# Performance work log

Hardware: AMD Instinct MI355X
Metric: run time of the kernel (lower is better)

## Reference

```python
import jax, jax.numpy as jnp
import numpy as np

NUM_AGENTS = 16


def setup_inputs() -> dict:
    key = jax.random.key(0)
    ks = jax.random.split(key, 9)
    B, N, C = 64, 1024, 512
    w_scale = 1.0 / np.sqrt(C)  # keep pre-softmax logits in a sane range
    return {
        "x": jax.random.normal(ks[0], (B, N, C), dtype=jnp.float32),
        "Wq": jax.random.normal(ks[1], (C, C), dtype=jnp.float32) * w_scale,
        "bq": jax.random.normal(ks[2], (C,), dtype=jnp.float32) * 0.02,
        "Wk": jax.random.normal(ks[3], (C, C), dtype=jnp.float32) * w_scale,
        "bk": jax.random.normal(ks[4], (C,), dtype=jnp.float32) * 0.02,
        "Wv": jax.random.normal(ks[5], (C, C), dtype=jnp.float32) * w_scale,
        "bv": jax.random.normal(ks[6], (C,), dtype=jnp.float32) * 0.02,
        "Wo": jax.random.normal(ks[7], (C, C), dtype=jnp.float32) * w_scale,
        "bo": jax.random.normal(ks[8], (C,), dtype=jnp.float32) * 0.02,
    }


def reference(x, Wq, bq, Wk, bk, Wv, bv, Wo, bo):
    B, N, C = x.shape
    M = NUM_AGENTS
    scale = C ** (-0.5)
    # torch nn.Linear: y = x @ W.T + b
    Q = jnp.einsum('bnc,dc->bnd', x, Wq) + bq  # [B,N,C]
    K = jnp.einsum('bnc,dc->bnd', x, Wk) + bk
    V = jnp.einsum('bnc,dc->bnd', x, Wv) + bv
    # adaptive_avg_pool1d over token dim; N % M == 0 -> mean over groups of N//M
    A = Q.reshape(B, M, N // M, C).mean(axis=2)  # [B,M,C]
    # stage 1: softmax(Q A^T)
    agent_tokens = jax.nn.softmax(jnp.einsum('bnc,bmc->bnm', Q, A) * scale, axis=-1)  # [B,N,M]
    # stage 2: softmax(A K^T) V
    agent_features = jax.nn.softmax(jnp.einsum('bmc,bnc->bmn', A, K) * scale, axis=-1)  # [B,M,N]
    agent_features = jnp.einsum('bmn,bnc->bmc', agent_features, V)  # [B,M,C]
    # combine
    agent_attn = jnp.einsum('bnm,bmc->bnc', agent_tokens, agent_features)  # [B,N,C]
    return jnp.einsum('bnc,dc->bnd', agent_attn, Wo) + bo
```

## Files before the change

### kernel.cpp

```cpp
#include <hip/hip_runtime.h>

#define BB 64
#define NN 1024
#define CC 512
#define MM 16
#define SCALE 0.04419417382415922f

__device__ __forceinline__ float dot4(float4 a, float4 b) {
  return a.x*b.x + a.y*b.y + a.z*b.z + a.w*b.w;
}
__device__ __forceinline__ void fma4(float4& acc, float s, float4 v) {
  acc.x += s*v.x; acc.y += s*v.y; acc.z += s*v.z; acc.w += s*v.w;
}

__global__ void k_pool2(const float* __restrict__ x, float* __restrict__ P) {
  __shared__ float4 tmp[128];
  int blk = blockIdx.x;
  int t = threadIdx.x;
  int c4 = t & 127, h = t >> 7;
  const float4* base = (const float4*)(x + (size_t)blk * 64 * CC);
  float4 a = {0.f,0.f,0.f,0.f};
  #pragma unroll 8
  for (int i = 0; i < 32; ++i) {
    float4 v = base[(size_t)(h*32 + i)*128 + c4];
    a.x += v.x; a.y += v.y; a.z += v.z; a.w += v.w;
  }
  if (h == 1) tmp[c4] = a;
  __syncthreads();
  if (h == 0) {
    float4 o = tmp[c4];
    const float inv = 1.0f/64.0f;
    float4 r = {(a.x+o.x)*inv, (a.y+o.y)*inv, (a.z+o.z)*inv, (a.w+o.w)*inv};
    ((float4*)P)[(size_t)blk*128 + c4] = r;
  }
}

__global__ __launch_bounds__(256) void k_gemm_nt3(const float* __restrict__ In,
    const float* __restrict__ W, const float* __restrict__ bias,
    float* __restrict__ Out) {
  __shared__ float4 As[8*128];
  int t = threadIdx.x;
  int rblk = blockIdx.y, dblk = blockIdx.x;
  const float4* In4 = (const float4*)In;
  #pragma unroll
  for (int k = 0; k < 4; ++k) {
    int i = k*256 + t;
    As[i] = In4[(size_t)(rblk*8 + (i>>7))*128 + (i&127)];
  }
  __syncthreads();
  int d = dblk*64 + (t & 63);
  int rr = t >> 6;
  const float4* Wr = (const float4*)W + (size_t)d*128;
  const float4* A0 = &As[(rr*2)*128];
  const float4* A1 = &As[(rr*2+1)*128];
  float acc0 = 0.f, acc1 = 0.f;
  #pragma unroll 4
  for (int c4 = 0; c4 < 128; ++c4) {
    float4 w = Wr[c4];
    acc0 += dot4(A0[c4], w);
    acc1 += dot4(A1[c4], w);
  }
  float bv = bias[d];
  int r0 = rblk*8 + rr*2;
  Out[(size_t)r0*CC + d] = acc0 + bv;
  Out[(size_t)(r0+1)*CC + d] = acc1 + bv;
}

__global__ void k_abqk(const float* __restrict__ A, const float* __restrict__ bq,
                       const float* __restrict__ bk, float* __restrict__ abq,
                       float* __restrict__ abk) {
  int bm = blockIdx.x, t = threadIdx.x;
  float sq = 0.f, sk = 0.f;
  for (int d = t; d < CC; d += 64) {
    float a = A[(size_t)bm*CC + d];
    sq += a*bq[d]; sk += a*bk[d];
  }
  #pragma unroll
  for (int off = 32; off >= 1; off >>= 1) {
    sq += __shfl_xor(sq, off);
    sk += __shfl_xor(sk, off);
  }
  if (t == 0) { abq[bm] = sq; abk[bm] = sk; }
}

__global__ __launch_bounds__(256) void k_gemm_nn3(const float* __restrict__ A,
    const float* __restrict__ Wq, const float* __restrict__ Wk,
    float* __restrict__ Aq, float* __restrict__ Ak) {
  __shared__ float As[4*512];
  int t = threadIdx.x;
  int rblk = blockIdx.y, cblk = blockIdx.x;
  const float4* A4 = (const float4*)A;
  float4* As4 = (float4*)As;
  #pragma unroll
  for (int k = 0; k < 2; ++k) {
    int i = k*256 + t;
    As4[i] = A4[(size_t)(rblk*4 + (i>>7))*128 + (i&127)];
  }
  __syncthreads();
  int c4 = cblk*64 + (t & 63);
  int rr = t >> 6;
  const float* Ar = &As[rr*512];
  const float4* Wq4 = (const float4*)Wq;
  const float4* Wk4 = (const float4*)Wk;
  float4 accq = {0.f,0.f,0.f,0.f}, acck = {0.f,0.f,0.f,0.f};
  #pragma unroll 8
  for (int d = 0; d < 512; ++d) {
    float a = Ar[d];
    fma4(accq, a, Wq4[(size_t)d*128 + c4]);
    fma4(acck, a, Wk4[(size_t)d*128 + c4]);
  }
  int row = rblk*4 + rr;
  ((float4*)Aq)[(size_t)row*128 + c4] = accq;
  ((float4*)Ak)[(size_t)row*128 + c4] = acck;
}

__global__ __launch_bounds__(128) void k_logits4(const float* __restrict__ x,
    const float* __restrict__ Aq, const float* __restrict__ Ak,
    float* __restrict__ Pq, float* __restrict__ Pk) {
  __shared__ float4 xs[128*17];
  int b = blockIdx.y, t = threadIdx.x, cz = blockIdx.z;
  int n0 = blockIdx.x*128;
  const float4* Aq4 = (const float4*)(Aq + (size_t)b*MM*CC);
  const float4* Ak4 = (const float4*)(Ak + (size_t)b*MM*CC);
  const float4* xg  = (const float4*)(x + ((size_t)b*NN + n0)*CC);
  float aq[MM], ak[MM];
  #pragma unroll
  for (int m = 0; m < MM; ++m) { aq[m] = 0.f; ak[m] = 0.f; }
  for (int ch = 0; ch < 2; ++ch) {
    __syncthreads();
    #pragma unroll
    for (int j = 0; j < 16; ++j) {
      int i = j*128 + t;
      int row = i >> 4, col = i & 15;
      xs[row*17 + col] = xg[(size_t)row*128 + cz*32 + ch*16 + col];
    }
    __syncthreads();
    int cb = cz*32 + ch*16;
    #pragma unroll 4
    for (int c4 = 0; c4 < 16; ++c4) {
      float4 xv = xs[t*17 + c4];
      #pragma unroll
      for (int m = 0; m < MM; ++m) {
        aq[m] += dot4(xv, Aq4[m*128 + cb + c4]);
        ak[m] += dot4(xv, Ak4[m*128 + cb + c4]);
      }
    }
  }
  int n = n0 + t;
  float4* Pq4 = (float4*)Pq + (((size_t)cz*BB + b)*NN + n)*4;
  float4* Pk4 = (float4*)Pk + (((size_t)cz*BB + b)*NN + n)*4;
  #pragma unroll
  for (int j = 0; j < 4; ++j) {
    float4 v = {aq[j*4+0], aq[j*4+1], aq[j*4+2], aq[j*4+3]};
    Pq4[j] = v;
    float4 w = {ak[j*4+0], ak[j*4+1], ak[j*4+2], ak[j*4+3]};
    Pk4[j] = w;
  }
}

__global__ __launch_bounds__(256) void k_sacc4(const float* __restrict__ x,
    const float* __restrict__ Pq, const float* __restrict__ Pk,
    const float* __restrict__ abq, const float* __restrict__ abk,
    float* __restrict__ PT, float* __restrict__ dpart,
    float* __restrict__ Spart) {
  __shared__ float Es[MM*128];
  __shared__ float4 comb[MM*128];
  __shared__ float ds2[128];
  int ns = blockIdx.x, b = blockIdx.y, t = threadIdx.x;
  int n0 = ns*128;
  if (t < 128) {
    int n = n0 + t;
    float4 s[4];
    #pragma unroll
    for (int j = 0; j < 4; ++j) s[j] = make_float4(0.f,0.f,0.f,0.f);
    #pragma unroll
    for (int cz = 0; cz < 4; ++cz) {
      const float4* Pk4 = (const float4*)Pk + (((size_t)cz*BB + b)*NN + n)*4;
      #pragma unroll
      for (int j = 0; j < 4; ++j) {
        float4 v = Pk4[j];
        s[j].x += v.x; s[j].y += v.y; s[j].z += v.z; s[j].w += v.w;
      }
    }
    #pragma unroll
    for (int j = 0; j < 4; ++j) {
      Es[(j*4+0)*128 + t] = expf(SCALE*(s[j].x + abk[b*MM + j*4+0]));
      Es[(j*4+1)*128 + t] = expf(SCALE*(s[j].y + abk[b*MM + j*4+1]));
      Es[(j*4+2)*128 + t] = expf(SCALE*(s[j].z + abk[b*MM + j*4+2]));
      Es[(j*4+3)*128 + t] = expf(SCALE*(s[j].w + abk[b*MM + j*4+3]));
    }
  } else {
    int n = n0 + (t - 128);
    float a[MM];
    #pragma unroll
    for (int m = 0; m < MM; ++m) a[m] = 0.f;
    #pragma unroll
    for (int cz = 0; cz < 4; ++cz) {
      const float4* Pq4 = (const float4*)Pq + (((size_t)cz*BB + b)*NN + n)*4;
      #pragma unroll
      for (int j = 0; j < 4; ++j) {
        float4 v = Pq4[j];
        a[j*4+0] += v.x; a[j*4+1] += v.y; a[j*4+2] += v.z; a[j*4+3] += v.w;
      }
    }
    float mx = -1e30f;
    #pragma unroll
    for (int m = 0; m < MM; ++m) {
      a[m] = SCALE*(a[m] + abq[b*MM + m]);
      mx = fmaxf(mx, a[m]);
    }
    float ssum = 0.f;
    #pragma unroll
    for (int m = 0; m < MM; ++m) { a[m] = expf(a[m]-mx); ssum += a[m]; }
    float inv = 1.0f/ssum;
    float4* PT4 = (float4*)PT + ((size_t)b*NN + n)*4;
    #pragma unroll
    for (int j = 0; j < 4; ++j) {
      float4 v = {a[j*4+0]*inv, a[j*4+1]*inv, a[j*4+2]*inv, a[j*4+3]*inv};
      PT4[j] = v;
    }
  }
  __syncthreads();
  if (t < 128) {
    int m = t >> 3, j = t & 7;
    float p = 0.f;
    #pragma unroll
    for (int i = 0; i < 16; ++i) p += Es[m*128 + j*16 + i];
    ds2[t] = p;
  }
  __syncthreads();
  if (t < MM) {
    float dsum = 0.f;
    #pragma unroll
    for (int j = 0; j < 8; ++j) dsum += ds2[t*8 + j];
    dpart[((size_t)ns*BB + b)*MM + t] = dsum;
  }
  int col = t & 127, h = t >> 7;
  float4 acc[MM];
  #pragma unroll
  for (int m = 0; m < MM; ++m) acc[m] = make_float4(0.f,0.f,0.f,0.f);
  const float4* xb = (const float4*)(x + ((size_t)b*NN + n0 + h*64)*CC);
  for (int nl = 0; nl < 64; ++nl) {
    float4 xv = xb[(size_t)nl*128 + col];
    #pragma unroll
    for (int m = 0; m < MM; ++m)
      fma4(acc[m], Es[m*128 + h*64 + nl], xv);
  }
  if (h == 1) {
    #pragma unroll
    for (int m = 0; m < MM; ++m) comb[m*128 + col] = acc[m];
  }
  __syncthreads();
  if (h == 0) {
    float4* Sp4 = (float4*)Spart;
    #pragma unroll
    for (int m = 0; m < MM; ++m) {
      float4 c = comb[m*128 + col];
      float4 r = {acc[m].x+c.x, acc[m].y+c.y, acc[m].z+c.z, acc[m].w+c.w};
      Sp4[(((size_t)ns*BB + b)*MM + m)*128 + col] = r;
    }
  }
}

__global__ void k_sreduce2(const float* __restrict__ Spart,
                           const float* __restrict__ dpart,
                           float* __restrict__ S) {
  int idx = blockIdx.x*256 + threadIdx.x;
  int row = idx >> 7;
  const float4* Sp4 = (const float4*)Spart;
  float4 a = {0.f,0.f,0.f,0.f};
  #pragma unroll
  for (int ns = 0; ns < 8; ++ns) {
    float4 v = Sp4[((size_t)ns*NN + row)*128 + (idx & 127)];
    a.x += v.x; a.y += v.y; a.z += v.z; a.w += v.w;
  }
  float d = 0.f;
  #pragma unroll
  for (int ns = 0; ns < 8; ++ns) d += dpart[(size_t)ns*NN + row];
  float inv = 1.0f/d;
  float4 r = {a.x*inv, a.y*inv, a.z*inv, a.w*inv};
  ((float4*)S)[idx] = r;
}

__global__ __launch_bounds__(128) void k_final4(const float* __restrict__ PT,
                                                const float* __restrict__ G,
                                                float* __restrict__ out) {
  int nc = blockIdx.x, b = blockIdx.y, t = threadIdx.x;
  float4 g[MM];
  const float4* G4 = (const float4*)(G + (size_t)b*MM*CC);
  #pragma unroll
  for (int m = 0; m < MM; ++m) g[m] = G4[m*128 + t];
  int n0 = nc*16;
  float4* out4 = (float4*)(out + ((size_t)b*NN + n0)*CC);
  const float* pt = PT + ((size_t)b*NN + n0)*MM;
  for (int i = 0; i < 16; ++i) {
    float4 o = {0.f,0.f,0.f,0.f};
    #pragma unroll
    for (int m = 0; m < MM; ++m) {
      float p = pt[i*MM + m];
      o.x += p*g[m].x; o.y += p*g[m].y; o.z += p*g[m].z; o.w += p*g[m].w;
    }
    out4[(size_t)i*128 + t] = o;
  }
}

extern "C" void kernel_launch(void* const* d_in, const int* in_sizes, int n_in,
                              void* d_out, int out_size, void* d_ws, size_t ws_size,
                              hipStream_t stream) {
  (void)in_sizes; (void)n_in; (void)out_size; (void)ws_size;
  const float* x  = (const float*)d_in[0];
  const float* Wq = (const float*)d_in[1];
  const float* bq = (const float*)d_in[2];
  const float* Wk = (const float*)d_in[3];
  const float* bk = (const float*)d_in[4];
  const float* Wv = (const float*)d_in[5];
  const float* bv = (const float*)d_in[6];
  const float* Wo = (const float*)d_in[7];
  const float* bo = (const float*)d_in[8];
  float* out = (float*)d_out;

  float* ws  = (float*)d_ws;
  float* P     = ws;
  float* A     = P  + 1024*512;
  float* Aq    = A  + 1024*512;
  float* Ak    = Aq + 1024*512;
  float* abq   = Ak + 1024*512;
  float* abk   = abq + 1024;
  float* PT    = abk + 1024;
  float* dpart = PT + 1024*1024;
  float* S     = dpart + 8*1024;
  float* AF    = S  + 1024*512;
  float* G     = AF + 1024*512;
  float* Spart = G  + 1024*512;
  float* Pq    = Spart + 8*1024*512;
  float* Pk    = Pq + 4*1024*1024/4*4;

  k_pool2<<<1024, 256, 0, stream>>>(x, P);
  k_gemm_nt3<<<dim3(8,128), 256, 0, stream>>>(P, Wq, bq, A);
  k_abqk<<<1024, 64, 0, stream>>>(A, bq, bk, abq, abk);
  k_gemm_nn3<<<dim3(2,256), 256, 0, stream>>>(A, Wq, Wk, Aq, Ak);
  k_logits4<<<dim3(8,64,4), 128, 0, stream>>>(x, Aq, Ak, Pq, Pk);
  k_sacc4<<<dim3(8,64), 256, 0, stream>>>(x, Pq, Pk, abq, abk, PT, dpart, Spart);
  k_sreduce2<<<512, 256, 0, stream>>>(Spart, dpart, S);
  k_gemm_nt3<<<dim3(8,128), 256, 0, stream>>>(S, Wv, bv, AF);
  k_gemm_nt3<<<dim3(8,128), 256, 0, stream>>>(AF, Wo, bo, G);
  k_final4<<<dim3(64,64), 128, 0, stream>>>(PT, G, out);
}
```

Baseline: 759.0 us.

## Fuse logits into agent accumulation, tile small GEMMs with split-K atomics

Merges the logits kernel into the agent-accumulation kernel, so each block computes per-token Q/K logits with shuffle reductions and no longer writes or reads the Pq/Pk partial buffers. The small GEMMs are rewritten as 64x64 shared-memory tiles with a 4-way split-K that accumulates through atomicAdd into buffers zeroed with memsets. The pooling and final kernels are also reshaped for more parallelism, with PT staged in shared memory. The intent is to cut x re-reads and intermediate global traffic, at the cost of atomic contention, extra memsets and nondeterministic summation order.

```diff
diff --git a/kernel.cpp b/kernel.cpp
--- a/kernel.cpp
+++ b/kernel.cpp
@@ -9,61 +9,91 @@
 __device__ __forceinline__ float dot4(float4 a, float4 b) {
   return a.x*b.x + a.y*b.y + a.z*b.z + a.w*b.w;
 }
-__device__ __forceinline__ void fma4(float4& acc, float s, float4 v) {
-  acc.x += s*v.x; acc.y += s*v.y; acc.z += s*v.z; acc.w += s*v.w;
-}
-
-__global__ void k_pool2(const float* __restrict__ x, float* __restrict__ P) {
-  __shared__ float4 tmp[128];
-  int blk = blockIdx.x;
-  int t = threadIdx.x;
-  int c4 = t & 127, h = t >> 7;
-  const float4* base = (const float4*)(x + (size_t)blk * 64 * CC);
+
+__global__ __launch_bounds__(128) void k_pool3(const float* __restrict__ x,
+                                               float* __restrict__ P) {
+  __shared__ float4 tmp[64];
+  int bm = blockIdx.x, ch = blockIdx.y, t = threadIdx.x;
+  int col = t & 63, p = t >> 6;
+  const float4* base = (const float4*)(x + (size_t)bm*64*CC) + ch*64;
   float4 a = {0.f,0.f,0.f,0.f};
   #pragma unroll 8
   for (int i = 0; i < 32; ++i) {
-    float4 v = base[(size_t)(h*32 + i)*128 + c4];
+    float4 v = base[(size_t)(p*32 + i)*128 + col];
     a.x += v.x; a.y += v.y; a.z += v.z; a.w += v.w;
   }
-  if (h == 1) tmp[c4] = a;
-  __syncthreads();
-  if (h == 0) {
-    float4 o = tmp[c4];
+  if (p == 1) tmp[col] = a;
+  __syncthreads();
+  if (p == 0) {
+    float4 o = tmp[col];
     const float inv = 1.0f/64.0f;
     float4 r = {(a.x+o.x)*inv, (a.y+o.y)*inv, (a.z+o.z)*inv, (a.w+o.w)*inv};
-    ((float4*)P)[(size_t)blk*128 + c4] = r;
-  }
-}
-
-__global__ __launch_bounds__(256) void k_gemm_nt3(const float* __restrict__ In,
+    ((float4*)P)[(size_t)bm*128 + ch*64 + col] = r;
+  }
+}
+
+__global__ __launch_bounds__(256) void k_gemm_nt4(const float* __restrict__ In,
     const float* __restrict__ W, const float* __restrict__ bias,
     float* __restrict__ Out) {
-  __shared__ float4 As[8*128];
+  __shared__ float Is[64*36];
+  __shared__ float Ws[64*36];
   int t = threadIdx.x;
-  int rblk = blockIdx.y, dblk = blockIdx.x;
+  int dblk = blockIdx.x, rblk = blockIdx.y, kz = blockIdx.z;
+  int td = t & 15, tr = t >> 4;
+  float acc[4][4];
+  #pragma unroll
+  for (int i = 0; i < 4; ++i)
+    #pragma unroll
+    for (int j = 0; j < 4; ++j) acc[i][j] = 0.f;
   const float4* In4 = (const float4*)In;
-  #pragma unroll
-  for (int k = 0; k < 4; ++k) {
-    int i = k*256 + t;
-    As[i] = In4[(size_t)(rblk*8 + (i>>7))*128 + (i&127)];
-  }
-  __syncthreads();
-  int d = dblk*64 + (t & 63);
-  int rr = t >> 6;
-  const float4* Wr = (const float4*)W + (size_t)d*128;
-  const float4* A0 = &As[(rr*2)*128];
-  const float4* A1 = &As[(rr*2+1)*128];
-  float acc0 = 0.f, acc1 = 0.f;
-  #pragma unroll 4
-  for (int c4 = 0; c4 < 128; ++c4) {
-    float4 w = Wr[c4];
-    acc0 += dot4(A0[c4], w);
-    acc1 += dot4(A1[c4], w);
-  }
-  float bv = bias[d];
-  int r0 = rblk*8 + rr*2;
-  Out[(size_t)r0*CC + d] = acc0 + bv;
-  Out[(size_t)(r0+1)*CC + d] = acc1 + bv;
+  const float4* W4  = (const float4*)W;
+  for (int chk = 0; chk < 4; ++chk) {
+    int kc = kz*32 + chk*8;
+    __syncthreads();
+    #pragma unroll
+    for (int p = 0; p < 2; ++p) {
+      int i = p*256 + t;
+      int r = i >> 3, cc = i & 7;
+      float4 v = In4[(size_t)(rblk*64 + r)*128 + kc + cc];
+      *(float4*)&Is[r*36 + cc*4] = v;
+      float4 w = W4[(size_t)(dblk*64 + r)*128 + kc + cc];
+      *(float4*)&Ws[r*36 + cc*4] = w;
+    }
+    __syncthreads();
+    #pragma unroll
+    for (int cc = 0; cc < 8; ++cc) {
+      float4 a0 = *(float4*)&Is[(tr*4+0)*36 + cc*4];
+      float4 a1 = *(float4*)&Is[(tr*4+1)*36 + cc*4];
+      float4 a2 = *(float4*)&Is[(tr*4+2)*36 + cc*4];
+      float4 a3 = *(float4*)&Is[(tr*4+3)*36 + cc*4];
+      float4 w0 = *(float4*)&Ws[(td*4+0)*36 + cc*4];
+      float4 w1 = *(float4*)&Ws[(td*4+1)*36 + cc*4];
+      float4 w2 = *(float4*)&Ws[(td*4+2)*36 + cc*4];
+      float4 w3 = *(float4*)&Ws[(td*4+3)*36 + cc*4];
+      acc[0][0] += dot4(a0,w0); acc[0][1] += dot4(a0,w1);
+      acc[0][2] += dot4(a0,w2); acc[0][3] += dot4(a0,w3);
+      acc[1][0] += dot4(a1,w0); acc[1][1] += dot4(a1,w1);
+      acc[1][2] += dot4(a1,w2); acc[1][3] += dot4(a1,w3);
+      acc[2][0] += dot4(a2,w0); acc[2][1] += dot4(a2,w1);
+      acc[2][2] += dot4(a2,w2); acc[2][3] += dot4(a2,w3);
+      acc[3][0] += dot4(a3,w0); acc[3][1] += dot4(a3,w1);
+      acc[3][2] += dot4(a3,w2); acc[3][3] += dot4(a3,w3);
+    }
+  }
+  int r0 = rblk*64 + tr*4, d0 = dblk*64 + td*4;
+  if (kz == 0) {
+    #pragma unroll
+    for (int j = 0; j < 4; ++j) {
+      float bj = bias[d0+j];
+      #pragma unroll
+      for (int i = 0; i < 4; ++i) acc[i][j] += bj;
+    }
+  }
+  #pragma unroll
+  for (int i = 0; i < 4; ++i)
+    #pragma unroll
+    for (int j = 0; j < 4; ++j)
+      atomicAdd(&Out[(size_t)(r0+i)*CC + d0 + j], acc[i][j]);
 }
 
 __global__ void k_abqk(const float* __restrict__ A, const float* __restrict__ bq,
@@ -106,118 +136,79 @@
   #pragma unroll 8
   for (int d = 0; d < 512; ++d) {
     float a = Ar[d];
-    fma4(accq, a, Wq4[(size_t)d*128 + c4]);
-    fma4(acck, a, Wk4[(size_t)d*128 + c4]);
+    float4 wq = Wq4[(size_t)d*128 + c4];
+    float4 wk = Wk4[(size_t)d*128 + c4];
+    accq.x += a*wq.x; accq.y += a*wq.y; accq.z += a*wq.z; accq.w += a*wq.w;
+    acck.x += a*wk.x; acck.y += a*wk.y; acck.z += a*wk.z; acck.w += a*wk.w;
   }
   int row = rblk*4 + rr;
   ((float4*)Aq)[(size_t)row*128 + c4] = accq;
   ((float4*)Ak)[(size_t)row*128 + c4] = acck;
 }
 
-__global__ __launch_bounds__(128) void k_logits4(const float* __restrict__ x,
+__global__ __launch_bounds__(256) void k_mega(const float* __restrict__ x,
     const float* __restrict__ Aq, const float* __restrict__ Ak,
-    float* __restrict__ Pq, float* __restrict__ Pk) {
-  __shared__ float4 xs[128*17];
-  int b = blockIdx.y, t = threadIdx.x, cz = blockIdx.z;
-  int n0 = blockIdx.x*128;
-  const float4* Aq4 = (const float4*)(Aq + (size_t)b*MM*CC);
-  const float4* Ak4 = (const float4*)(Ak + (size_t)b*MM*CC);
-  const float4* xg  = (const float4*)(x + ((size_t)b*NN + n0)*CC);
-  float aq[MM], ak[MM];
-  #pragma unroll
-  for (int m = 0; m < MM; ++m) { aq[m] = 0.f; ak[m] = 0.f; }
-  for (int ch = 0; ch < 2; ++ch) {
-    __syncthreads();
-    #pragma unroll
-    for (int j = 0; j < 16; ++j) {
-      int i = j*128 + t;
-      int row = i >> 4, col = i & 15;
-      xs[row*17 + col] = xg[(size_t)row*128 + cz*32 + ch*16 + col];
-    }
-    __syncthreads();
-    int cb = cz*32 + ch*16;
-    #pragma unroll 4
-    for (int c4 = 0; c4 < 16; ++c4) {
-      float4 xv = xs[t*17 + c4];
-      #pragma unroll
-      for (int m = 0; m < MM; ++m) {
-        aq[m] += dot4(xv, Aq4[m*128 + cb + c4]);
-        ak[m] += dot4(xv, Ak4[m*128 + cb + c4]);
-      }
-    }
-  }
-  int n = n0 + t;
-  float4* Pq4 = (float4*)Pq + (((size_t)cz*BB + b)*NN + n)*4;
-  float4* Pk4 = (float4*)Pk + (((size_t)cz*BB + b)*NN + n)*4;
-  #pragma unroll
-  for (int j = 0; j < 4; ++j) {
-    float4 v = {aq[j*4+0], aq[j*4+1], aq[j*4+2], aq[j*4+3]};
-    Pq4[j] = v;
-    float4 w = {ak[j*4+0], ak[j*4+1], ak[j*4+2], ak[j*4+3]};
-    Pk4[j] = w;
-  }
-}
-
-__global__ __launch_bounds__(256) void k_sacc4(const float* __restrict__ x,
-    const float* __restrict__ Pq, const float* __restrict__ Pk,
     const float* __restrict__ abq, const float* __restrict__ abk,
     float* __restrict__ PT, float* __restrict__ dpart,
     float* __restrict__ Spart) {
-  __shared__ float Es[MM*128];
-  __shared__ float4 comb[MM*128];
+  __shared__ float Es[64*16];
   __shared__ float ds2[128];
   int ns = blockIdx.x, b = blockIdx.y, t = threadIdx.x;
-  int n0 = ns*128;
-  if (t < 128) {
-    int n = n0 + t;
-    float4 s[4];
-    #pragma unroll
-    for (int j = 0; j < 4; ++j) s[j] = make_float4(0.f,0.f,0.f,0.f);
-    #pragma unroll
-    for (int cz = 0; cz < 4; ++cz) {
-      const float4* Pk4 = (const float4*)Pk + (((size_t)cz*BB + b)*NN + n)*4;
+  int n0 = ns*64;
+  int ci = t & 15, tw = t >> 4;
+  const float4* Aq4 = (const float4*)(Aq + (size_t)b*MM*CC);
+  const float4* Ak4 = (const float4*)(Ak + (size_t)b*MM*CC);
+  for (int pass = 0; pass < 4; ++pass) {
+    int tok = pass*16 + tw;
+    int n = n0 + tok;
+    const float4* xr = (const float4*)(x + ((size_t)b*NN + n)*CC);
+    float aq[MM], ak[MM];
+    #pragma unroll
+    for (int m = 0; m < MM; ++m) { aq[m] = 0.f; ak[m] = 0.f; }
+    #pragma unroll 4
+    for (int k = 0; k < 8; ++k) {
+      float4 xv = xr[k*16 + ci];
+      #pragma unroll
+      for (int m = 0; m < MM; ++m) {
+        aq[m] += dot4(xv, Aq4[m*128 + k*16 + ci]);
+        ak[m] += dot4(xv, Ak4[m*128 + k*16 + ci]);
+      }
+    }
+    #pragma unroll
+    for (int off = 1; off < 16; off <<= 1) {
+      #pragma unroll
+      for (int m = 0; m < MM; ++m) {
+        aq[m] += __shfl_xor(aq[m], off);
+        ak[m] += __shfl_xor(ak[m], off);
+      }
+    }
+    if (ci == 0) {
+      float mx = -1e30f;
+      #pragma unroll
+      for (int m = 0; m < MM; ++m) {
+        aq[m] = SCALE*(aq[m] + abq[b*MM + m]);
+        mx = fmaxf(mx, aq[m]);
+      }
+      float s = 0.f;
+      #pragma unroll
+      for (int m = 0; m < MM; ++m) { aq[m] = expf(aq[m]-mx); s += aq[m]; }
+      float inv = 1.0f/s;
+      float4* PT4 = (float4*)(PT + ((size_t)b*NN + n)*MM);
       #pragma unroll
       for (int j = 0; j < 4; ++j) {
-        float4 v = Pk4[j];
-        s[j].x += v.x; s[j].y += v.y; s[j].z += v.z; s[j].w += v.w;
-      }
-    }
-    #pragma unroll
-    for (int j = 0; j < 4; ++j) {
-      Es[(j*4+0)*128 + t] = expf(SCALE*(s[j].x + abk[b*MM + j*4+0]));
-      Es[(j*4+1)*128 + t] = expf(SCALE*(s[j].y + abk[b*MM + j*4+1]));
-      Es[(j*4+2)*128 + t] = expf(SCALE*(s[j].z + abk[b*MM + j*4+2]));
-      Es[(j*4+3)*128 + t] = expf(SCALE*(s[j].w + abk[b*MM + j*4+3]));
-    }
-  } else {
-    int n = n0 + (t - 128);
-    float a[MM];
-    #pragma unroll
-    for (int m = 0; m < MM; ++m) a[m] = 0.f;
-    #pragma unroll
-    for (int cz = 0; cz < 4; ++cz) {
-      const float4* Pq4 = (const float4*)Pq + (((size_t)cz*BB + b)*NN + n)*4;
+        float4 v = {aq[j*4+0]*inv, aq[j*4+1]*inv, aq[j*4+2]*inv, aq[j*4+3]*inv};
+        PT4[j] = v;
+      }
+      float e[MM];
+      #pragma unroll
+      for (int m = 0; m < MM; ++m)
+        e[m] = expf(SCALE*(ak[m] + abk[b*MM + m]));
+      float4* er = (float4*)&Es[tok*MM];
       #pragma unroll
       for (int j = 0; j < 4; ++j) {
-        float4 v = Pq4[j];
-        a[j*4+0] += v.x; a[j*4+1] += v.y; a[j*4+2] += v.z; a[j*4+3] += v.w;
-      }
-    }
-    float mx = -1e30f;
-    #pragma unroll
-    for (int m = 0; m < MM; ++m) {
-      a[m] = SCALE*(a[m] + abq[b*MM + m]);
-      mx = fmaxf(mx, a[m]);
-    }
-    float ssum = 0.f;
-    #pragma unroll
-    for (int m = 0; m < MM; ++m) { a[m] = expf(a[m]-mx); ssum += a[m]; }
-    float inv = 1.0f/ssum;
-    float4* PT4 = (float4*)PT + ((size_t)b*NN + n)*4;
-    #pragma unroll
-    for (int j = 0; j < 4; ++j) {
-      float4 v = {a[j*4+0]*inv, a[j*4+1]*inv, a[j*4+2]*inv, a[j*4+3]*inv};
-      PT4[j] = v;
+        float4 v = {e[j*4+0], e[j*4+1], e[j*4+2], e[j*4+3]};
+        er[j] = v;
+      }
     }
   }
   __syncthreads();
@@ -225,44 +216,37 @@
     int m = t >> 3, j = t & 7;
     float p = 0.f;
     #pragma unroll
-    for (int i = 0; i < 16; ++i) p += Es[m*128 + j*16 + i];
-    ds2[t] = p;
+    for (int i = 0; i < 8; ++i) p += Es[(j*8 + i)*MM + m];
+    ds2[m*8 + j] = p;
   }
   __syncthreads();
   if (t < MM) {
-    float dsum = 0.f;
-    #pragma unroll
-    for (int j = 0; j < 8; ++j) dsum += ds2[t*8 + j];
-    dpart[((size_t)ns*BB + b)*MM + t] = dsum;
-  }
-  int col = t & 127, h = t >> 7;
-  float4 acc[MM];
-  #pragma unroll
-  for (int m = 0; m < MM; ++m) acc[m] = make_float4(0.f,0.f,0.f,0.f);
-  const float4* xb = (const float4*)(x + ((size_t)b*NN + n0 + h*64)*CC);
+    float d = 0.f;
+    #pragma unroll
+    for (int j = 0; j < 8; ++j) d += ds2[t*8 + j];
+    dpart[(size_t)ns*NN + b*MM + t] = d;
+  }
+  int c2 = t;
+  float2 acc[MM];
+  #pragma unroll
+  for (int m = 0; m < MM; ++m) acc[m] = make_float2(0.f, 0.f);
+  const float2* xb = (const float2*)(x + ((size_t)b*NN + n0)*CC);
+  #pragma unroll 4
   for (int nl = 0; nl < 64; ++nl) {
-    float4 xv = xb[(size_t)nl*128 + col];
-    #pragma unroll
-    for (int m = 0; m < MM; ++m)
-      fma4(acc[m], Es[m*128 + h*64 + nl], xv);
-  }
-  if (h == 1) {
-    #pragma unroll
-    for (int m = 0; m < MM; ++m) comb[m*128 + col] = acc[m];
-  }
-  __syncthreads();
-  if (h == 0) {
-    float4* Sp4 = (float4*)Spart;
+    float2 xv = xb[(size_t)nl*256 + c2];
     #pragma unroll
     for (int m = 0; m < MM; ++m) {
-      float4 c = comb[m*128 + col];
-      float4 r = {acc[m].x+c.x, acc[m].y+c.y, acc[m].z+c.z, acc[m].w+c.w};
-      Sp4[(((size_t)ns*BB + b)*MM + m)*128 + col] = r;
-    }
-  }
-}
-
-__global__ void k_sreduce2(const float* __restrict__ Spart,
+      float e = Es[nl*MM + m];
+      acc[m].x += e*xv.x; acc[m].y += e*xv.y;
+    }
+  }
+  float2* Sp2 = (float2*)Spart;
+  #pragma unroll
+  for (int m = 0; m < MM; ++m)
+    Sp2[(((size_t)ns*BB + b)*MM + m)*256 + c2] = acc[m];
+}
+
+__global__ void k_sreduce3(const float* __restrict__ Spart,
                            const float* __restrict__ dpart,
                            float* __restrict__ S) {
   int idx = blockIdx.x*256 + threadIdx.x;
@@ -270,37 +254,41 @@
   const float4* Sp4 = (const float4*)Spart;
   float4 a = {0.f,0.f,0.f,0.f};
   #pragma unroll
-  for (int ns = 0; ns < 8; ++ns) {
+  for (int ns = 0; ns < 16; ++ns) {
     float4 v = Sp4[((size_t)ns*NN + row)*128 + (idx & 127)];
     a.x += v.x; a.y += v.y; a.z += v.z; a.w += v.w;
   }
   float d = 0.f;
   #pragma unroll
-  for (int ns = 0; ns < 8; ++ns) d += dpart[(size_t)ns*NN + row];
+  for (int ns = 0; ns < 16; ++ns) d += dpart[(size_t)ns*NN + row];
   float inv = 1.0f/d;
   float4 r = {a.x*inv, a.y*inv, a.z*inv, a.w*inv};
   ((float4*)S)[idx] = r;
 }
 
-__global__ __launch_bounds__(128) void k_final4(const float* __restrict__ PT,
+__global__ __launch_bounds__(256) void k_final5(const float* __restrict__ PT,
                                                 const float* __restrict__ G,
                                                 float* __restrict__ out) {
+  __shared__ float ps[32*MM];
   int nc = blockIdx.x, b = blockIdx.y, t = threadIdx.x;
+  int col = t & 127, h = t >> 7;
+  int n0 = nc*32;
+  if (t < 128)
+    ((float4*)ps)[t] = ((const float4*)(PT + ((size_t)b*NN + n0)*MM))[t];
   float4 g[MM];
   const float4* G4 = (const float4*)(G + (size_t)b*MM*CC);
   #pragma unroll
-  for (int m = 0; m < MM; ++m) g[m] = G4[m*128 + t];
-  int n0 = nc*16;
-  float4* out4 = (float4*)(out + ((size_t)b*NN + n0)*CC);
-  const float* pt = PT + ((size_t)b*NN + n0)*MM;
+  for (int m = 0; m < MM; ++m) g[m] = G4[m*128 + col];
+  __syncthreads();
+  float4* out4 = (float4*)(out + ((size_t)b*NN + n0 + h*16)*CC);
   for (int i = 0; i < 16; ++i) {
     float4 o = {0.f,0.f,0.f,0.f};
     #pragma unroll
     for (int m = 0; m < MM; ++m) {
-      float p = pt[i*MM + m];
+      float p = ps[(h*16 + i)*MM + m];
       o.x += p*g[m].x; o.y += p*g[m].y; o.z += p*g[m].z; o.w += p*g[m].w;
     }
-    out4[(size_t)i*128 + t] = o;
+    out4[(size_t)i*128 + col] = o;
   }
 }
 
@@ -328,21 +316,22 @@
   float* abk   = abq + 1024;
   float* PT    = abk + 1024;
   float* dpart = PT + 1024*1024;
-  float* S     = dpart + 8*1024;
+  float* S     = dpart + 16*1024;
   float* AF    = S  + 1024*512;
   float* G     = AF + 1024*512;
   float* Spart = G  + 1024*512;
-  float* Pq    = Spart + 8*1024*512;
-  float* Pk    = Pq + 4*1024*1024/4*4;
-
-  k_pool2<<<1024, 256, 0, stream>>>(x, P);
-  k_gemm_nt3<<<dim3(8,128), 256, 0, stream>>>(P, Wq, bq, A);
+
+  hipMemsetAsync(A,  0, (size_t)1024*512*sizeof(float), stream);
+  hipMemsetAsync(AF, 0, (size_t)1024*512*sizeof(float), stream);
+  hipMemsetAsync(G,  0, (size_t)1024*512*sizeof(float), stream);
+
+  k_pool3<<<dim3(1024,2), 128, 0, stream>>>(x, P);
+  k_gemm_nt4<<<dim3(8,16,4), 256, 0, stream>>>(P, Wq, bq, A);
   k_abqk<<<1024, 64, 0, stream>>>(A, bq, bk, abq, abk);
   k_gemm_nn3<<<dim3(2,256), 256, 0, stream>>>(A, Wq, Wk, Aq, Ak);
-  k_logits4<<<dim3(8,64,4), 128, 0, stream>>>(x, Aq, Ak, Pq, Pk);
-  k_sacc4<<<dim3(8,64), 256, 0, stream>>>(x, Pq, Pk, abq, abk, PT, dpart, Spart);
-  k_sreduce2<<<512, 256, 0, stream>>>(Spart, dpart, S);
-  k_gemm_nt3<<<dim3(8,128), 256, 0, stream>>>(S, Wv, bv, AF);
-  k_gemm_nt3<<<dim3(8,128), 256, 0, stream>>>(AF, Wo, bo, G);
-  k_final4<<<dim3(64,64), 128, 0, stream>>>(PT, G, out);
-}
+  k_mega<<<dim3(16,64), 256, 0, stream>>>(x, Aq, Ak, abq, abk, PT, dpart, Spart);
+  k_sreduce3<<<512, 256, 0, stream>>>(Spart, dpart, S);
+  k_gemm_nt4<<<dim3(8,16,4), 256, 0, stream>>>(S, Wv, bv, AF);
+  k_gemm_nt4<<<dim3(8,16,4), 256, 0, stream>>>(AF, Wo, bo, G);
+  k_final5<<<dim3(32,64), 256, 0, stream>>>(PT, G, out);
+}
```

After: 741.9 us. 1.02x faster.
